# Performance work log

Measured on AMD Instinct MI355X. Metric: run time of the kernel, lower is better.

The kernel has to match this reference:

```python
import jax, jax.numpy as jnp
import numpy as np

D = 512            # token_dim * num_heads
TOKEN_DIM = 256
SCALE = TOKEN_DIM ** (-0.5)
EPS = 1e-12        # torch F.normalize eps
FIDX = (0, 1, 1)   # original bug: out_rv uses final_myo


def l2norm(x, axis):
    n = jnp.sqrt(jnp.sum(x * x, axis=axis, keepdims=True))
    return x / jnp.maximum(n, EPS)


def setup_inputs() -> dict:
    key = jax.random.key(0)
    ks = jax.random.split(key, 16)
    B, N = 16, 1024
    s = 0.02
    return {
        "x_lv": jax.random.normal(ks[0], (B, N, D), jnp.float32),
        "x_myo": jax.random.normal(ks[1], (B, N, D), jnp.float32),
        "x_rv": jax.random.normal(ks[2], (B, N, D), jnp.float32),
        # stacked per-branch params: branch 0=lv, 1=myo, 2=rv
        "Wq": jax.random.normal(ks[3], (3, D, D), jnp.float32) * s,
        "bq": jax.random.normal(ks[4], (3, D), jnp.float32) * s,
        "Wk": jax.random.normal(ks[5], (3, D, D), jnp.float32) * s,
        "bk": jax.random.normal(ks[6], (3, D), jnp.float32) * s,
        "wg": jax.random.normal(ks[7], (3, D, 1), jnp.float32),
        "Wp": jax.random.normal(ks[8], (3, 3, D, D), jnp.float32) * s,  # [branch, key_src]
        "bp": jax.random.normal(ks[9], (3, 3, D), jnp.float32) * s,
        "Wf": jax.random.normal(ks[10], (3, D, TOKEN_DIM), jnp.float32) * s,
        "bf": jax.random.normal(ks[11], (3, TOKEN_DIM), jnp.float32) * s,
    }


def reference(x_lv, x_myo, x_rv, Wq, bq, Wk, bk, wg, Wp, bp, Wf, bf):
    X = (x_lv, x_myo, x_rv)
    # projections + L2 normalize over feature dim
    Q = [l2norm(X[m] @ Wq[m] + bq[m], axis=-1) for m in range(3)]  # [B,N,D]
    K = [l2norm(X[m] @ Wk[m] + bk[m], axis=-1) for m in range(3)]  # [B,N,D]
    outs = []
    for m in range(3):
        A = l2norm((Q[m] @ wg[m]) * SCALE, axis=1)       # [B,N,1], normed over seq
        G = jnp.sum(A * Q[m], axis=1)[:, None, :]        # [B,1,D] (broadcast repeat)
        acc = Q[m]
        for j in range(3):
            acc = acc + (G * K[j]) @ Wp[m, j] + bp[m, j]
        outs.append(acc @ Wf[FIDX[m]] + bf[FIDX[m]])     # [B,N,token_dim]
    return tuple(outs)
```

## Files before the change

kernel.cpp:

```cpp
#include <hip/hip_runtime.h>
#include <hip/hip_bf16.h>

typedef __hip_bfloat16 bf16;
typedef __attribute__((ext_vector_type(8))) short short8;
typedef __attribute__((ext_vector_type(4))) float f32x4;

#define SCALE_F 0.0625f

__device__ __forceinline__ float b2f(short s) {
  union { float f; unsigned int u; } x;
  x.u = ((unsigned int)(unsigned short)s) << 16;
  return x.f;
}
__device__ __forceinline__ unsigned short f2bu(float f) {
  __hip_bfloat16 h = __float2bfloat16(f);
  unsigned short u;
  __builtin_memcpy(&u, &h, 2);
  return u;
}
__device__ __forceinline__ void store_out(float* p, float v) { *p = v; }
__device__ __forceinline__ void store_out(bf16* p, float v) { *p = __float2bfloat16(v); }

typedef __attribute__((address_space(3))) void lds_void;
typedef __attribute__((address_space(1))) void gbl_void;

__device__ __forceinline__ void lds_load16(void* l, const void* g) {
  __builtin_amdgcn_global_load_lds((const gbl_void*)g, (lds_void*)l, 16, 0, 0);
}

template<typename OutT>
__device__ __forceinline__ void gemm256_tile(
    const bf16* A0, const bf16* A1, const bf16* A2, const bf16* A3, int ldA,
    const bf16* Bt, int ldB, OutT* C, int ldC, const float* bias,
    int K, int row0, int col0)
{
  __shared__ bf16 Abuf0[256 * 64], Abuf1[256 * 64];
  __shared__ bf16 Bbuf0[256 * 64], Bbuf1[256 * 64];
  const int tid = threadIdx.x;
  const int lane = tid & 63, w = tid >> 6;
  const int wm = w >> 2, wn = w & 3;
  const int lr = lane & 15, hi = lane >> 4;

  const int stageR = tid >> 3;
  const int stageC = ((tid & 7) ^ (stageR & 7)) << 3;
  const bf16* Bg0 = Bt + (size_t)(col0 + stageR) * ldB + stageC;

  auto stage = [&](int bsel, int k0) {
    const int seg = k0 >> 9;
    const bf16* Aseg = (seg == 0) ? A0 : (seg == 1) ? A1 : (seg == 2) ? A2 : A3;
    const bf16* Ag = Aseg + (size_t)(row0 + stageR) * ldA + (k0 & 511) + stageC;
    const bf16* Bg = Bg0 + k0;
    bf16* Al = (bsel ? Abuf1 : Abuf0) + tid * 8;
    bf16* Bl = (bsel ? Bbuf1 : Bbuf0) + tid * 8;
#pragma unroll
    for (int q = 0; q < 4; ++q) {
      lds_load16(Al + q * 4096, Ag + (size_t)q * 64 * ldA);
      lds_load16(Bl + q * 4096, Bg + (size_t)q * 64 * ldB);
    }
  };

  const int aoffb = (wm * 128 + lr) * 128;
  const int boffb = (wn * 64 + lr) * 128;
  const int s0 = ((hi ^ (lr & 7)) << 4);
  const int s1 = (((4 + hi) ^ (lr & 7)) << 4);

  f32x4 acc[8][4];
#pragma unroll
  for (int i = 0; i < 8; ++i)
#pragma unroll
    for (int j = 0; j < 4; ++j) acc[i][j] = (f32x4){0.f, 0.f, 0.f, 0.f};

  const int nt = K >> 6;
  stage(0, 0);
  stage(1, 64);
  asm volatile("s_waitcnt vmcnt(8)" ::: "memory");
  __builtin_amdgcn_s_barrier();

  for (int t = 0; t < nt; ++t) {
    const char* Ab = (const char*)((t & 1) ? Abuf1 : Abuf0);
    const char* Bb = (const char*)((t & 1) ? Bbuf1 : Bbuf0);
    short8 ra[8], rb[4], ra2[8], rb2[4];
#pragma unroll
    for (int fr = 0; fr < 8; ++fr) ra[fr] = *(const short8*)(Ab + aoffb + fr * 2048 + s0);
#pragma unroll
    for (int fq = 0; fq < 4; ++fq) rb[fq] = *(const short8*)(Bb + boffb + fq * 2048 + s0);
    __builtin_amdgcn_s_setprio(1);
#pragma unroll
    for (int fr = 0; fr < 8; ++fr)
#pragma unroll
      for (int fq = 0; fq < 4; ++fq)
        acc[fr][fq] = __builtin_amdgcn_mfma_f32_16x16x32_bf16(ra[fr], rb[fq], acc[fr][fq], 0, 0, 0);
    __builtin_amdgcn_s_setprio(0);
#pragma unroll
    for (int fr = 0; fr < 8; ++fr) ra2[fr] = *(const short8*)(Ab + aoffb + fr * 2048 + s1);
#pragma unroll
    for (int fq = 0; fq < 4; ++fq) rb2[fq] = *(const short8*)(Bb + boffb + fq * 2048 + s1);
    asm volatile("s_waitcnt lgkmcnt(0)" ::: "memory");
    __builtin_amdgcn_s_barrier();
    if (t + 2 < nt) stage(t & 1, (t + 2) << 6);
    __builtin_amdgcn_s_setprio(1);
#pragma unroll
    for (int fr = 0; fr < 8; ++fr)
#pragma unroll
      for (int fq = 0; fq < 4; ++fq)
        acc[fr][fq] = __builtin_amdgcn_mfma_f32_16x16x32_bf16(ra2[fr], rb2[fq], acc[fr][fq], 0, 0, 0);
    __builtin_amdgcn_s_setprio(0);
    if (t + 1 < nt) {
      if (t + 2 < nt) asm volatile("s_waitcnt vmcnt(8)" ::: "memory");
      else            asm volatile("s_waitcnt vmcnt(0)" ::: "memory");
      __builtin_amdgcn_s_barrier();
    }
  }

#pragma unroll
  for (int fr = 0; fr < 8; ++fr) {
    const int rowb = row0 + wm * 128 + fr * 16 + hi * 4;
#pragma unroll
    for (int fq = 0; fq < 4; ++fq) {
      const int col = col0 + wn * 64 + fq * 16 + lr;
      const float bv = bias ? bias[col] : 0.f;
      f32x4 v = acc[fr][fq];
#pragma unroll
      for (int r = 0; r < 4; ++r)
        store_out(&C[(size_t)(rowb + r) * ldC + col], v[r] + bv);
    }
  }
}

template<typename OutT>
__device__ __forceinline__ void gemm_tile(
    const bf16* A0, const bf16* A1, const bf16* A2, const bf16* A3,
    int ldA, const bf16* Bt, int ldB, OutT* C, int ldC,
    const float* bias, int K, int row0, int col0)
{
  __shared__ bf16 As[128 * 32];
  __shared__ bf16 Bs[128 * 32];
  const int t = threadIdx.x;
  const int lane = t & 63;
  const int w = t >> 6;
  const int wm = w >> 1, wn = w & 1;
  const int lr = lane & 15, hi = lane >> 4;
  const int rA = t >> 2;
  const int kA = (t & 3) * 8;

  f32x4 acc[4][4];
#pragma unroll
  for (int i = 0; i < 4; ++i)
#pragma unroll
    for (int j = 0; j < 4; ++j) acc[i][j] = (f32x4){0.f, 0.f, 0.f, 0.f};

  const int nk = K >> 5;
  for (int kt = 0; kt < nk; ++kt) {
    const int k0 = kt << 5;
    const int s = k0 >> 9;
    const bf16* Aseg = (s == 0) ? A0 : (s == 1) ? A1 : (s == 2) ? A2 : A3;
    const int kl = (k0 & 511) + kA;
    __syncthreads();
    lds_load16(&As[t * 8],        Aseg + (size_t)(row0 + rA) * ldA + kl);
    lds_load16(&As[2048 + t * 8], Aseg + (size_t)(row0 + 64 + rA) * ldA + kl);
    lds_load16(&Bs[t * 8],        Bt + (size_t)(col0 + rA) * ldB + k0 + kA);
    lds_load16(&Bs[2048 + t * 8], Bt + (size_t)(col0 + 64 + rA) * ldB + k0 + kA);
    __syncthreads();
    short8 af[4], bfr[4];
#pragma unroll
    for (int f = 0; f < 4; ++f)
      af[f] = *(const short8*)&As[(wm * 64 + f * 16 + lr) * 32 + hi * 8];
#pragma unroll
    for (int f = 0; f < 4; ++f)
      bfr[f] = *(const short8*)&Bs[(wn * 64 + f * 16 + lr) * 32 + hi * 8];
#pragma unroll
    for (int i = 0; i < 4; ++i)
#pragma unroll
      for (int j = 0; j < 4; ++j)
        acc[i][j] = __builtin_amdgcn_mfma_f32_16x16x32_bf16(af[i], bfr[j], acc[i][j], 0, 0, 0);
  }

#pragma unroll
  for (int i = 0; i < 4; ++i) {
    const int rowb = row0 + wm * 64 + i * 16 + hi * 4;
#pragma unroll
    for (int j = 0; j < 4; ++j) {
      const int col = col0 + wn * 64 + j * 16 + lr;
      const float bv = bias ? bias[col] : 0.f;
      f32x4 v = acc[i][j];
#pragma unroll
      for (int r = 0; r < 4; ++r)
        store_out(&C[(size_t)(rowb + r) * ldC + col], v[r] + bv);
    }
  }
}

__global__ __launch_bounds__(256) void k_convert_x(
    const float* __restrict__ x0, const float* __restrict__ x1,
    const float* __restrict__ x2, bf16* __restrict__ xbf)
{
  const long long i = (long long)blockIdx.x * 256 + threadIdx.x;
  const int tt = (int)(i / 2097152);
  const long long e = i - (long long)tt * 2097152;
  const float4* src = (const float4*)(tt == 0 ? x0 : tt == 1 ? x1 : x2);
  float4 v = src[e];
  ushort4 o;
  o.x = f2bu(v.x); o.y = f2bu(v.y); o.z = f2bu(v.z); o.w = f2bu(v.w);
  ((ushort4*)xbf)[i] = o;
}

__global__ __launch_bounds__(256) void k_transpose(
    const float* __restrict__ in, bf16* __restrict__ out, int R, int C)
{
  const int tilesC = C >> 6;
  const int tr = (blockIdx.x / tilesC) << 6;
  const int tc = (blockIdx.x % tilesC) << 6;
  const size_t base = (size_t)blockIdx.y * R * C;
  __shared__ unsigned short tile[64][72];
  const int rr = threadIdx.x >> 4;
  const int cc = (threadIdx.x & 15) << 2;
#pragma unroll
  for (int p = 0; p < 4; ++p) {
    const int r = rr + (p << 4);
    float4 v = *(const float4*)&in[base + (size_t)(tr + r) * C + tc + cc];
    tile[cc + 0][r] = f2bu(v.x);
    tile[cc + 1][r] = f2bu(v.y);
    tile[cc + 2][r] = f2bu(v.z);
    tile[cc + 3][r] = f2bu(v.w);
  }
  __syncthreads();
#pragma unroll
  for (int p = 0; p < 4; ++p) {
    const int r = rr + (p << 4);
    ushort4 o;
    o.x = tile[r][cc + 0];
    o.y = tile[r][cc + 1];
    o.z = tile[r][cc + 2];
    o.w = tile[r][cc + 3];
    *(ushort4*)&out[base + (size_t)(tc + r) * R + tr + cc] = o;
  }
}

__global__ __launch_bounds__(256) void k_copy_bf16(
    const float* __restrict__ in, bf16* __restrict__ out)
{
  const long long i = (long long)blockIdx.x * 256 + threadIdx.x;
  float4 v = ((const float4*)in)[i];
  ushort4 o;
  o.x = f2bu(v.x); o.y = f2bu(v.y); o.z = f2bu(v.z); o.w = f2bu(v.w);
  ((ushort4*)out)[i] = o;
}

__global__ __launch_bounds__(256) void k_bprime(
    const float* __restrict__ bp, const float* __restrict__ Wf,
    const float* __restrict__ bfv, float* __restrict__ bpr)
{
  const int m = blockIdx.x;
  const int dc = blockIdx.y;
  const int n = threadIdx.x;
  const int fi = (m == 0) ? 0 : 1;
  float s = (dc == 0) ? bfv[fi * 256 + n] : 0.f;
  for (int d = dc * 64; d < dc * 64 + 64; ++d) {
    float b3 = bp[(m * 3 + 0) * 512 + d] + bp[(m * 3 + 1) * 512 + d] +
               bp[(m * 3 + 2) * 512 + d];
    s += b3 * Wf[(size_t)fi * 512 * 256 + (size_t)d * 256 + n];
  }
  atomicAdd(&bpr[m * 256 + n], s);
}

__global__ __launch_bounds__(512, 2) void k_gemm1(
    const bf16* __restrict__ Xbf, const bf16* __restrict__ WT,
    const float* __restrict__ bq, const float* __restrict__ bk,
    bf16* __restrict__ QK)
{
  const int bid = blockIdx.x;
  const int swz = (bid & 7) * 96 + (bid >> 3);
  const int m = swz >> 8;
  const int rem = swz & 255;
  const int tm = rem >> 2;
  const int tn = (rem >> 1) & 1;
  const int qk = rem & 1;
  const int inst = qk ? (m + 3) : m;
  const bf16* A = Xbf + (size_t)m * (16384 * 512);
  const bf16* B = WT + (size_t)inst * (512 * 512);
  const float* bias = (qk ? bk : bq) + m * 512;
  bf16* C = QK + (size_t)inst * (16384 * 512);
  gemm256_tile<bf16>(A, A, A, A, 512, B, 512, C, 512, bias, 512, tm * 256, tn * 256);
}

__global__ __launch_bounds__(256) void k_gemm_wpf(
    const bf16* __restrict__ WfT, const bf16* __restrict__ Wpbf,
    float* __restrict__ WpfT)
{
  const int inst = blockIdx.y;
  const int m = inst / 3;
  const int fi = (m == 0) ? 0 : 1;
  const int tm = blockIdx.x >> 2, tn = blockIdx.x & 3;
  const bf16* A = WfT + (size_t)fi * (256 * 512);
  const bf16* B = Wpbf + (size_t)inst * (512 * 512);
  float* C = WpfT + (size_t)inst * (256 * 512);
  gemm_tile<float>(A, A, A, A, 512, B, 512, C, 512, nullptr, 512, tm * 128, tn * 128);
}

__global__ __launch_bounds__(512, 2) void k_gemm2(
    const bf16* __restrict__ QK, const bf16* __restrict__ W2T,
    const float* __restrict__ bpr, float* __restrict__ out)
{
  const int bid = blockIdx.x;
  const int swz = (bid & 7) * 24 + (bid >> 3);
  const int b = swz / 12;
  const int rem = swz % 12;
  const int m = rem >> 2;
  const int tm = rem & 3;
  const int e = m * 16 + b;
  const bf16* A0 = QK + ((size_t)m * 16384 + (size_t)b * 1024) * 512;
  const bf16* A1 = QK + ((size_t)(3 * 16384) + (size_t)b * 1024) * 512;
  const bf16* A2 = QK + ((size_t)(4 * 16384) + (size_t)b * 1024) * 512;
  const bf16* A3 = QK + ((size_t)(5 * 16384) + (size_t)b * 1024) * 512;
  const bf16* Bt = W2T + (size_t)e * (256 * 2048);
  float* C = out + (size_t)e * (1024 * 256);
  gemm256_tile<float>(A0, A1, A2, A3, 512, Bt, 2048, C, 256, bpr + m * 256, 2048,
                      tm * 256, 0);
}

__global__ __launch_bounds__(256) void k_norm(
    bf16* __restrict__ QK, const float* __restrict__ wg, float* __restrict__ qdot)
{
  const int row = blockIdx.x * 4 + (threadIdx.x >> 6);
  const int lane = threadIdx.x & 63;
  bf16* p = QK + (size_t)row * 512 + lane * 8;
  short8 v = *(const short8*)p;
  float f[8];
  float ss = 0.f;
#pragma unroll
  for (int i = 0; i < 8; ++i) { f[i] = b2f(v[i]); ss += f[i] * f[i]; }
#pragma unroll
  for (int o = 32; o; o >>= 1) ss += __shfl_xor(ss, o);
  const float inv = 1.f / fmaxf(sqrtf(ss), 1e-12f);
  short8 ov;
#pragma unroll
  for (int i = 0; i < 8; ++i) ov[i] = (short)f2bu(f[i] * inv);
  *(short8*)p = ov;
  const int tt = row >> 14;
  if (tt < 3) {
    const float* wgm = wg + (size_t)tt * 512 + lane * 8;
    float dot = 0.f;
#pragma unroll
    for (int i = 0; i < 8; ++i) dot += f[i] * wgm[i];
    dot *= inv;
#pragma unroll
    for (int o = 32; o; o >>= 1) dot += __shfl_xor(dot, o);
    if (lane == 0) qdot[row] = dot;
  }
}

__global__ __launch_bounds__(256) void k_G(
    const float* __restrict__ qdot, const bf16* __restrict__ QK, float* __restrict__ G)
{
  const int e = blockIdx.x;
  const int m = e >> 4, b = e & 15;
  const int d0 = blockIdx.y << 6;
  __shared__ float Al[1024];
  __shared__ float red[4];
  __shared__ float Gp[4][64];
  const int t = threadIdx.x;
  const float* qd = qdot + (size_t)m * 16384 + (size_t)b * 1024;
  float ss = 0.f;
#pragma unroll
  for (int i = 0; i < 4; ++i) {
    float x = qd[t + i * 256] * SCALE_F;
    Al[t + i * 256] = x;
    ss += x * x;
  }
#pragma unroll
  for (int o = 32; o; o >>= 1) ss += __shfl_xor(ss, o);
  if ((t & 63) == 0) red[t >> 6] = ss;
  __syncthreads();
  const float inv = 1.f / fmaxf(sqrtf(red[0] + red[1] + red[2] + red[3]), 1e-12f);

  const int d = d0 + (t & 63);
  const int q = t >> 6;
  const bf16* Qb = QK + ((size_t)m * 16384 + (size_t)b * 1024) * 512 + d;
  float g = 0.f;
  for (int n = q * 256; n < q * 256 + 256; ++n)
    g += Al[n] * b2f(*(const short*)&Qb[(size_t)n * 512]);
  Gp[q][t & 63] = g;
  __syncthreads();
  if (t < 64)
    G[(size_t)e * 512 + d0 + t] = (Gp[0][t] + Gp[1][t] + Gp[2][t] + Gp[3][t]) * inv;
}

__global__ __launch_bounds__(256) void k_w2t(
    const bf16* __restrict__ WfT, const float* __restrict__ WpfT,
    const float* __restrict__ G, bf16* __restrict__ W2T)
{
  const int e = blockIdx.x;
  const int m = e >> 4;
  const int fi = (m == 0) ? 0 : 1;
  const int t = threadIdx.x;
  bf16* out = W2T + (size_t)e * (256 * 2048);
  __shared__ float Gl[512];
  Gl[t] = G[(size_t)e * 512 + t];
  Gl[t + 256] = G[(size_t)e * 512 + t + 256];
  __syncthreads();
  const int k = t * 8;
  for (int nr = 0; nr < 16; ++nr) {
    const int n = blockIdx.y * 16 + nr;
    if (k < 512) {
      *(short8*)&out[(size_t)n * 2048 + k] =
          *(const short8*)&WfT[((size_t)fi * 256 + n) * 512 + k];
    } else {
      const int j = (k >> 9) - 1;
      const int d = k & 511;
      const float* src = WpfT + (((size_t)(m * 3 + j) * 256 + n) * 512 + d);
      short8 o;
#pragma unroll
      for (int i = 0; i < 8; ++i) o[i] = (short)f2bu(Gl[d + i] * src[i]);
      *(short8*)&out[(size_t)n * 2048 + k] = o;
    }
  }
}

extern "C" void kernel_launch(void* const* d_in, const int* in_sizes, int n_in,
                              void* d_out, int out_size, void* d_ws, size_t ws_size,
                              hipStream_t stream) {
  const float* x_lv = (const float*)d_in[0];
  const float* x_myo = (const float*)d_in[1];
  const float* x_rv = (const float*)d_in[2];
  const float* Wq = (const float*)d_in[3];
  const float* bq = (const float*)d_in[4];
  const float* Wk = (const float*)d_in[5];
  const float* bk = (const float*)d_in[6];
  const float* wg = (const float*)d_in[7];
  const float* Wp = (const float*)d_in[8];
  const float* bp = (const float*)d_in[9];
  const float* Wf = (const float*)d_in[10];
  const float* bfv = (const float*)d_in[11];
  float* out = (float*)d_out;

  char* ws = (char*)d_ws;
  bf16* QK    = (bf16*)(ws);
  bf16* Xbf   = (bf16*)(ws + 100663296);
  bf16* WT    = (bf16*)(ws + 150994944);
  bf16* Wpbf  = (bf16*)(ws + 154140672);
  bf16* WfT   = (bf16*)(ws + 158859264);
  float* WpfT = (float*)(ws + 159383552);
  float* qdot = (float*)(ws + 164102144);
  float* G    = (float*)(ws + 164298752);
  float* bpr  = (float*)(ws + 164397056);
  bf16* W2T   = Xbf;

  k_convert_x<<<24576, 256, 0, stream>>>(x_lv, x_myo, x_rv, Xbf);
  k_transpose<<<dim3(64, 3), 256, 0, stream>>>(Wq, WT, 512, 512);
  k_transpose<<<dim3(64, 3), 256, 0, stream>>>(Wk, WT + 3 * 512 * 512, 512, 512);
  k_transpose<<<dim3(32, 2), 256, 0, stream>>>(Wf, WfT, 512, 256);
  k_copy_bf16<<<2304, 256, 0, stream>>>(Wp, Wpbf);
  hipMemsetAsync(bpr, 0, 3 * 256 * sizeof(float), stream);
  k_bprime<<<dim3(3, 8), 256, 0, stream>>>(bp, Wf, bfv, bpr);

  k_gemm1<<<768, 512, 0, stream>>>(Xbf, WT, bq, bk, QK);

  k_norm<<<24576, 256, 0, stream>>>(QK, wg, qdot);

  k_gemm_wpf<<<dim3(8, 9), 256, 0, stream>>>(WfT, Wpbf, WpfT);

  k_G<<<dim3(48, 8), 256, 0, stream>>>(qdot, QK, G);

  k_w2t<<<dim3(48, 16), 256, 0, stream>>>(WfT, WpfT, G, W2T);

  k_gemm2<<<192, 512, 0, stream>>>(QK, W2T, bpr, out);
}
```

Measured before the change: 379.8 us.

## Fuse fp32-to-bf16 input conversion into gemm1 and retile gemm2 to 128x128

Removes the separate pass that converts x to bf16. gemm1 now loads the fp32 activations into registers, converts them, and writes bf16 into LDS through a software-pipelined prefetch, which avoids writing and rereading a 48MB bf16 copy. gemm2 moves from 256x256 tiles with 512 threads (192 blocks) to 128x128 tiles with 256 threads (768 blocks), so more blocks can spread across the CUs. The cost is that the fp32 A loads double gemm1's global read bytes for A and go through registers, and the smaller gemm2 tiles reuse each loaded tile less.

```diff
diff --git a/kernel.cpp b/kernel.cpp
--- a/kernel.cpp
+++ b/kernel.cpp
@@ -28,17 +28,148 @@
   __builtin_amdgcn_global_load_lds((const gbl_void*)g, (lds_void*)l, 16, 0, 0);
 }
 
-template<typename OutT>
-__device__ __forceinline__ void gemm256_tile(
-    const bf16* A0, const bf16* A1, const bf16* A2, const bf16* A3, int ldA,
-    const bf16* Bt, int ldB, OutT* C, int ldC, const float* bias,
-    int K, int row0, int col0)
+__device__ __forceinline__ void gemm256_xf32(
+    const float* __restrict__ Af, int ldA,
+    const bf16* __restrict__ Bt, int ldB,
+    bf16* C, int ldC, const float* bias, int row0, int col0)
 {
   __shared__ bf16 Abuf0[256 * 64], Abuf1[256 * 64];
   __shared__ bf16 Bbuf0[256 * 64], Bbuf1[256 * 64];
   const int tid = threadIdx.x;
   const int lane = tid & 63, w = tid >> 6;
   const int wm = w >> 2, wn = w & 3;
+  const int lr = lane & 15, hi = lane >> 4;
+
+  const int stageR = tid >> 3;
+  const int cNat   = (tid & 7) << 3;
+  const int cSwz   = ((tid & 7) ^ (stageR & 7)) << 3;
+  const float* Ag0 = Af + (size_t)(row0 + stageR) * ldA + cNat;
+  const bf16*  Bg0 = Bt + (size_t)(col0 + stageR) * ldB + cSwz;
+  const int AwOff = stageR * 64 + cSwz;
+
+  float4 prefE[8], prefO[8];
+  auto issueA = [&](float4 (&dst)[8], int k0) {
+#pragma unroll
+    for (int q = 0; q < 4; ++q) {
+      const float* p = Ag0 + (size_t)(q * 64) * ldA + k0;
+      dst[q * 2 + 0] = *(const float4*)(p);
+      dst[q * 2 + 1] = *(const float4*)(p + 4);
+    }
+  };
+  auto writeA = [&](const float4 (&src)[8], bf16* Al) {
+#pragma unroll
+    for (int q = 0; q < 4; ++q) {
+      float4 v0 = src[q * 2 + 0], v1 = src[q * 2 + 1];
+      short8 o;
+      o[0] = (short)f2bu(v0.x); o[1] = (short)f2bu(v0.y);
+      o[2] = (short)f2bu(v0.z); o[3] = (short)f2bu(v0.w);
+      o[4] = (short)f2bu(v1.x); o[5] = (short)f2bu(v1.y);
+      o[6] = (short)f2bu(v1.z); o[7] = (short)f2bu(v1.w);
+      *(short8*)&Al[AwOff + q * 4096] = o;
+    }
+  };
+  auto stageB = [&](int bsel, int k0) {
+    bf16* Bl = (bsel ? Bbuf1 : Bbuf0) + tid * 8;
+    const bf16* Bg = Bg0 + k0;
+#pragma unroll
+    for (int q = 0; q < 4; ++q)
+      lds_load16(Bl + q * 4096, Bg + (size_t)(q * 64) * ldB);
+  };
+
+  const int aoffb = (wm * 128 + lr) * 128;
+  const int boffb = (wn * 64 + lr) * 128;
+  const int s0 = ((hi ^ (lr & 7)) << 4);
+  const int s1 = (((4 + hi) ^ (lr & 7)) << 4);
+
+  f32x4 acc[8][4];
+#pragma unroll
+  for (int i = 0; i < 8; ++i)
+#pragma unroll
+    for (int j = 0; j < 4; ++j) acc[i][j] = (f32x4){0.f, 0.f, 0.f, 0.f};
+
+  issueA(prefE, 0);
+  issueA(prefO, 64);
+  stageB(0, 0);
+  stageB(1, 64);
+  writeA(prefE, Abuf0);
+  issueA(prefE, 128);
+  writeA(prefO, Abuf1);
+  asm volatile("s_waitcnt vmcnt(12)" ::: "memory");
+  asm volatile("s_waitcnt lgkmcnt(0)" ::: "memory");
+  __builtin_amdgcn_s_barrier();
+
+#pragma unroll
+  for (int t = 0; t < 8; ++t) {
+    if (t + 3 < 8) {
+      if (((t + 3) & 1) == 0) issueA(prefE, (t + 3) * 64);
+      else                    issueA(prefO, (t + 3) * 64);
+    }
+    const char* Ab = (const char*)((t & 1) ? Abuf1 : Abuf0);
+    const char* Bb = (const char*)((t & 1) ? Bbuf1 : Bbuf0);
+    short8 ra[8], rb[4], ra2[8], rb2[4];
+#pragma unroll
+    for (int fr = 0; fr < 8; ++fr) ra[fr] = *(const short8*)(Ab + aoffb + fr * 2048 + s0);
+#pragma unroll
+    for (int fq = 0; fq < 4; ++fq) rb[fq] = *(const short8*)(Bb + boffb + fq * 2048 + s0);
+    __builtin_amdgcn_s_setprio(1);
+#pragma unroll
+    for (int fr = 0; fr < 8; ++fr)
+#pragma unroll
+      for (int fq = 0; fq < 4; ++fq)
+        acc[fr][fq] = __builtin_amdgcn_mfma_f32_16x16x32_bf16(ra[fr], rb[fq], acc[fr][fq], 0, 0, 0);
+    __builtin_amdgcn_s_setprio(0);
+#pragma unroll
+    for (int fr = 0; fr < 8; ++fr) ra2[fr] = *(const short8*)(Ab + aoffb + fr * 2048 + s1);
+#pragma unroll
+    for (int fq = 0; fq < 4; ++fq) rb2[fq] = *(const short8*)(Bb + boffb + fq * 2048 + s1);
+    asm volatile("s_waitcnt lgkmcnt(0)" ::: "memory");
+    __builtin_amdgcn_s_barrier();
+    if (t + 2 < 8) {
+      if ((t & 1) == 0) writeA(prefE, Abuf0);
+      else              writeA(prefO, Abuf1);
+      stageB(t & 1, (t + 2) * 64);
+    }
+    __builtin_amdgcn_s_setprio(1);
+#pragma unroll
+    for (int fr = 0; fr < 8; ++fr)
+#pragma unroll
+      for (int fq = 0; fq < 4; ++fq)
+        acc[fr][fq] = __builtin_amdgcn_mfma_f32_16x16x32_bf16(ra2[fr], rb2[fq], acc[fr][fq], 0, 0, 0);
+    __builtin_amdgcn_s_setprio(0);
+    if (t + 1 < 8) {
+      if (t + 3 < 8)      asm volatile("s_waitcnt vmcnt(12)" ::: "memory");
+      else if (t + 2 < 8) asm volatile("s_waitcnt vmcnt(4)"  ::: "memory");
+      else                asm volatile("s_waitcnt vmcnt(0)"  ::: "memory");
+      __builtin_amdgcn_s_barrier();
+    }
+  }
+
+#pragma unroll
+  for (int fr = 0; fr < 8; ++fr) {
+    const int rowb = row0 + wm * 128 + fr * 16 + hi * 4;
+#pragma unroll
+    for (int fq = 0; fq < 4; ++fq) {
+      const int col = col0 + wn * 64 + fq * 16 + lr;
+      const float bv = bias[col];
+      f32x4 v = acc[fr][fq];
+#pragma unroll
+      for (int r = 0; r < 4; ++r)
+        store_out(&C[(size_t)(rowb + r) * ldC + col], v[r] + bv);
+    }
+  }
+}
+
+template<typename OutT>
+__device__ __forceinline__ void gemm128p(
+    const bf16* A0, const bf16* A1, const bf16* A2, const bf16* A3, int ldA,
+    const bf16* Bt, int ldB, OutT* C, int ldC, const float* bias,
+    int K, int row0, int col0)
+{
+  __shared__ bf16 Abuf0[128 * 64], Abuf1[128 * 64];
+  __shared__ bf16 Bbuf0[128 * 64], Bbuf1[128 * 64];
+  const int tid = threadIdx.x;
+  const int lane = tid & 63, w = tid >> 6;
+  const int wm = w >> 1, wn = w & 1;
   const int lr = lane & 15, hi = lane >> 4;
 
   const int stageR = tid >> 3;
@@ -54,19 +185,19 @@
     bf16* Bl = (bsel ? Bbuf1 : Bbuf0) + tid * 8;
 #pragma unroll
     for (int q = 0; q < 4; ++q) {
-      lds_load16(Al + q * 4096, Ag + (size_t)q * 64 * ldA);
-      lds_load16(Bl + q * 4096, Bg + (size_t)q * 64 * ldB);
+      lds_load16(Al + q * 2048, Ag + (size_t)(q * 32) * ldA);
+      lds_load16(Bl + q * 2048, Bg + (size_t)(q * 32) * ldB);
     }
   };
 
-  const int aoffb = (wm * 128 + lr) * 128;
+  const int aoffb = (wm * 64 + lr) * 128;
   const int boffb = (wn * 64 + lr) * 128;
   const int s0 = ((hi ^ (lr & 7)) << 4);
   const int s1 = (((4 + hi) ^ (lr & 7)) << 4);
 
-  f32x4 acc[8][4];
-#pragma unroll
-  for (int i = 0; i < 8; ++i)
+  f32x4 acc[4][4];
+#pragma unroll
+  for (int i = 0; i < 4; ++i)
 #pragma unroll
     for (int j = 0; j < 4; ++j) acc[i][j] = (f32x4){0.f, 0.f, 0.f, 0.f};
 
@@ -79,20 +210,20 @@
   for (int t = 0; t < nt; ++t) {
     const char* Ab = (const char*)((t & 1) ? Abuf1 : Abuf0);
     const char* Bb = (const char*)((t & 1) ? Bbuf1 : Bbuf0);
-    short8 ra[8], rb[4], ra2[8], rb2[4];
-#pragma unroll
-    for (int fr = 0; fr < 8; ++fr) ra[fr] = *(const short8*)(Ab + aoffb + fr * 2048 + s0);
+    short8 ra[4], rb[4], ra2[4], rb2[4];
+#pragma unroll
+    for (int fr = 0; fr < 4; ++fr) ra[fr] = *(const short8*)(Ab + aoffb + fr * 2048 + s0);
 #pragma unroll
     for (int fq = 0; fq < 4; ++fq) rb[fq] = *(const short8*)(Bb + boffb + fq * 2048 + s0);
     __builtin_amdgcn_s_setprio(1);
 #pragma unroll
-    for (int fr = 0; fr < 8; ++fr)
+    for (int fr = 0; fr < 4; ++fr)
 #pragma unroll
       for (int fq = 0; fq < 4; ++fq)
         acc[fr][fq] = __builtin_amdgcn_mfma_f32_16x16x32_bf16(ra[fr], rb[fq], acc[fr][fq], 0, 0, 0);
     __builtin_amdgcn_s_setprio(0);
 #pragma unroll
-    for (int fr = 0; fr < 8; ++fr) ra2[fr] = *(const short8*)(Ab + aoffb + fr * 2048 + s1);
+    for (int fr = 0; fr < 4; ++fr) ra2[fr] = *(const short8*)(Ab + aoffb + fr * 2048 + s1);
 #pragma unroll
     for (int fq = 0; fq < 4; ++fq) rb2[fq] = *(const short8*)(Bb + boffb + fq * 2048 + s1);
     asm volatile("s_waitcnt lgkmcnt(0)" ::: "memory");
@@ -100,7 +231,7 @@
     if (t + 2 < nt) stage(t & 1, (t + 2) << 6);
     __builtin_amdgcn_s_setprio(1);
 #pragma unroll
-    for (int fr = 0; fr < 8; ++fr)
+    for (int fr = 0; fr < 4; ++fr)
 #pragma unroll
       for (int fq = 0; fq < 4; ++fq)
         acc[fr][fq] = __builtin_amdgcn_mfma_f32_16x16x32_bf16(ra2[fr], rb2[fq], acc[fr][fq], 0, 0, 0);
@@ -113,8 +244,8 @@
   }
 
 #pragma unroll
-  for (int fr = 0; fr < 8; ++fr) {
-    const int rowb = row0 + wm * 128 + fr * 16 + hi * 4;
+  for (int fr = 0; fr < 4; ++fr) {
+    const int rowb = row0 + wm * 64 + fr * 16 + hi * 4;
 #pragma unroll
     for (int fq = 0; fq < 4; ++fq) {
       const int col = col0 + wn * 64 + fq * 16 + lr;
@@ -129,8 +260,7 @@
 
 template<typename OutT>
 __device__ __forceinline__ void gemm_tile(
-    const bf16* A0, const bf16* A1, const bf16* A2, const bf16* A3,
-    int ldA, const bf16* Bt, int ldB, OutT* C, int ldC,
+    const bf16* A0, int ldA, const bf16* Bt, int ldB, OutT* C, int ldC,
     const float* bias, int K, int row0, int col0)
 {
   __shared__ bf16 As[128 * 32];
@@ -152,12 +282,9 @@
   const int nk = K >> 5;
   for (int kt = 0; kt < nk; ++kt) {
     const int k0 = kt << 5;
-    const int s = k0 >> 9;
-    const bf16* Aseg = (s == 0) ? A0 : (s == 1) ? A1 : (s == 2) ? A2 : A3;
-    const int kl = (k0 & 511) + kA;
     __syncthreads();
-    lds_load16(&As[t * 8],        Aseg + (size_t)(row0 + rA) * ldA + kl);
-    lds_load16(&As[2048 + t * 8], Aseg + (size_t)(row0 + 64 + rA) * ldA + kl);
+    lds_load16(&As[t * 8],        A0 + (size_t)(row0 + rA) * ldA + k0 + kA);
+    lds_load16(&As[2048 + t * 8], A0 + (size_t)(row0 + 64 + rA) * ldA + k0 + kA);
     lds_load16(&Bs[t * 8],        Bt + (size_t)(col0 + rA) * ldB + k0 + kA);
     lds_load16(&Bs[2048 + t * 8], Bt + (size_t)(col0 + 64 + rA) * ldB + k0 + kA);
     __syncthreads();
@@ -188,20 +315,6 @@
         store_out(&C[(size_t)(rowb + r) * ldC + col], v[r] + bv);
     }
   }
-}
-
-__global__ __launch_bounds__(256) void k_convert_x(
-    const float* __restrict__ x0, const float* __restrict__ x1,
-    const float* __restrict__ x2, bf16* __restrict__ xbf)
-{
-  const long long i = (long long)blockIdx.x * 256 + threadIdx.x;
-  const int tt = (int)(i / 2097152);
-  const long long e = i - (long long)tt * 2097152;
-  const float4* src = (const float4*)(tt == 0 ? x0 : tt == 1 ? x1 : x2);
-  float4 v = src[e];
-  ushort4 o;
-  o.x = f2bu(v.x); o.y = f2bu(v.y); o.z = f2bu(v.z); o.w = f2bu(v.w);
-  ((ushort4*)xbf)[i] = o;
 }
 
 __global__ __launch_bounds__(256) void k_transpose(
@@ -264,7 +377,8 @@
 }
 
 __global__ __launch_bounds__(512, 2) void k_gemm1(
-    const bf16* __restrict__ Xbf, const bf16* __restrict__ WT,
+    const float* __restrict__ x0, const float* __restrict__ x1,
+    const float* __restrict__ x2, const bf16* __restrict__ WT,
     const float* __restrict__ bq, const float* __restrict__ bk,
     bf16* __restrict__ QK)
 {
@@ -276,11 +390,11 @@
   const int tn = (rem >> 1) & 1;
   const int qk = rem & 1;
   const int inst = qk ? (m + 3) : m;
-  const bf16* A = Xbf + (size_t)m * (16384 * 512);
+  const float* A = (m == 0) ? x0 : (m == 1) ? x1 : x2;
   const bf16* B = WT + (size_t)inst * (512 * 512);
   const float* bias = (qk ? bk : bq) + m * 512;
   bf16* C = QK + (size_t)inst * (16384 * 512);
-  gemm256_tile<bf16>(A, A, A, A, 512, B, 512, C, 512, bias, 512, tm * 256, tn * 256);
+  gemm256_xf32(A, 512, B, 512, C, 512, bias, tm * 256, tn * 256);
 }
 
 __global__ __launch_bounds__(256) void k_gemm_wpf(
@@ -294,28 +408,27 @@
   const bf16* A = WfT + (size_t)fi * (256 * 512);
   const bf16* B = Wpbf + (size_t)inst * (512 * 512);
   float* C = WpfT + (size_t)inst * (256 * 512);
-  gemm_tile<float>(A, A, A, A, 512, B, 512, C, 512, nullptr, 512, tm * 128, tn * 128);
-}
-
-__global__ __launch_bounds__(512, 2) void k_gemm2(
+  gemm_tile<float>(A, 512, B, 512, C, 512, nullptr, 512, tm * 128, tn * 128);
+}
+
+__global__ __launch_bounds__(256, 2) void k_gemm2(
     const bf16* __restrict__ QK, const bf16* __restrict__ W2T,
     const float* __restrict__ bpr, float* __restrict__ out)
 {
   const int bid = blockIdx.x;
-  const int swz = (bid & 7) * 24 + (bid >> 3);
-  const int b = swz / 12;
-  const int rem = swz % 12;
-  const int m = rem >> 2;
-  const int tm = rem & 3;
-  const int e = m * 16 + b;
+  const int swz = (bid & 7) * 96 + (bid >> 3);
+  const int e = swz >> 4;
+  const int tm = (swz >> 1) & 7;
+  const int tn = swz & 1;
+  const int m = e / 16, b = e & 15;
   const bf16* A0 = QK + ((size_t)m * 16384 + (size_t)b * 1024) * 512;
   const bf16* A1 = QK + ((size_t)(3 * 16384) + (size_t)b * 1024) * 512;
   const bf16* A2 = QK + ((size_t)(4 * 16384) + (size_t)b * 1024) * 512;
   const bf16* A3 = QK + ((size_t)(5 * 16384) + (size_t)b * 1024) * 512;
   const bf16* Bt = W2T + (size_t)e * (256 * 2048);
   float* C = out + (size_t)e * (1024 * 256);
-  gemm256_tile<float>(A0, A1, A2, A3, 512, Bt, 2048, C, 256, bpr + m * 256, 2048,
-                      tm * 256, 0);
+  gemm128p<float>(A0, A1, A2, A3, 512, Bt, 2048, C, 256, bpr + m * 256, 2048,
+                  tm * 128, tn * 128);
 }
 
 __global__ __launch_bounds__(256) void k_norm(
@@ -435,7 +548,7 @@
 
   char* ws = (char*)d_ws;
   bf16* QK    = (bf16*)(ws);
-  bf16* Xbf   = (bf16*)(ws + 100663296);
+  bf16* W2T   = (bf16*)(ws + 100663296);
   bf16* WT    = (bf16*)(ws + 150994944);
   bf16* Wpbf  = (bf16*)(ws + 154140672);
   bf16* WfT   = (bf16*)(ws + 158859264);
@@ -443,9 +556,7 @@
   float* qdot = (float*)(ws + 164102144);
   float* G    = (float*)(ws + 164298752);
   float* bpr  = (float*)(ws + 164397056);
-  bf16* W2T   = Xbf;
-
-  k_convert_x<<<24576, 256, 0, stream>>>(x_lv, x_myo, x_rv, Xbf);
+
   k_transpose<<<dim3(64, 3), 256, 0, stream>>>(Wq, WT, 512, 512);
   k_transpose<<<dim3(64, 3), 256, 0, stream>>>(Wk, WT + 3 * 512 * 512, 512, 512);
   k_transpose<<<dim3(32, 2), 256, 0, stream>>>(Wf, WfT, 512, 256);
@@ -453,7 +564,7 @@
   hipMemsetAsync(bpr, 0, 3 * 256 * sizeof(float), stream);
   k_bprime<<<dim3(3, 8), 256, 0, stream>>>(bp, Wf, bfv, bpr);
 
-  k_gemm1<<<768, 512, 0, stream>>>(Xbf, WT, bq, bk, QK);
+  k_gemm1<<<768, 512, 0, stream>>>(x_lv, x_myo, x_rv, WT, bq, bk, QK);
 
   k_norm<<<24576, 256, 0, stream>>>(QK, wg, qdot);
 
@@ -463,5 +574,5 @@
 
   k_w2t<<<dim3(48, 16), 256, 0, stream>>>(WfT, WpfT, G, W2T);
 
-  k_gemm2<<<192, 512, 0, stream>>>(QK, W2T, bpr, out);
-}
+  k_gemm2<<<768, 256, 0, stream>>>(QK, W2T, bpr, out);
+}
```

Result: slower. 388.8 us (+2.4%).
